# Performance work log

Hardware: AMD Instinct MI355X
Metric: run time of the kernel (lower is better)

Reference implementation:

```python
import jax, jax.numpy as jnp
import numpy as np

B, L, D = 64, 1024, 64  # (batch*heads, seq_len, head_dim)


def setup_inputs() -> dict:
    key = jax.random.key(0)
    kq, kk, kv = jax.random.split(key, 3)
    q = jax.random.normal(kq, (B, L, D), dtype=jnp.float32)
    k = jax.random.normal(kk, (B, L, D), dtype=jnp.float32)
    v = jax.random.normal(kv, (B, L, D), dtype=jnp.float32)
    scale = jnp.float32(1.0 / np.sqrt(D))  # standard 1/sqrt(d_head)
    return {"q": q, "k": k, "v": v, "scale": scale}


def reference(q, k, v, scale):
    # attention = bmm(q, k^T) * scale  -> [B, L, L]
    attention = jnp.einsum("bqd,bkd->bqk", q, k) * scale
    # softmax over dim=2 (keys); dropout p=0.0 is identity
    attention = jax.nn.softmax(attention, axis=2)
    # context = bmm(attention, v) -> [B, L, D]
    context = jnp.einsum("bqk,bkd->bqd", attention, v)
    return (context, attention)
```

## Files before the change

### kernel.cpp

```cpp
#include <hip/hip_runtime.h>
#include <hip/hip_bf16.h>

typedef __bf16 bf16x8 __attribute__((ext_vector_type(8)));
typedef float  f32x4  __attribute__((ext_vector_type(4)));

#define NB 64
#define LL 1024
#define DD 64
#define HK 512
#define PSTR 36

#define LSUM_LDS  (LL * DD * 2)
#define MAIN_LDS  (2 * HK * DD * 2 + 8 * 16 * PSTR * 4)

#define WS_VT_OFF 0
#define WS_RL_OFF ((size_t)8 * 1024 * 1024)
#define WS_NEED   (WS_RL_OFF + (size_t)NB * LL * 4)

#if __has_builtin(__builtin_amdgcn_exp2f)
#define EXP2(x) __builtin_amdgcn_exp2f(x)
#else
#define EXP2(x) exp2f(x)
#endif

__global__ __launch_bounds__(256)
void preconvert_v(const float* __restrict__ v, __bf16* __restrict__ vt) {
  const int blk = blockIdx.x, tid = threadIdx.x;
  const int b = blk >> 4, t = blk & 15;
  __shared__ float tile[64][65];
  const float* src = v + ((size_t)b * LL + t * 64) * DD;
  for (int i = tid; i < 64 * 16; i += 256) {
    const int row = i >> 4, c4 = (i & 15) * 4;
    f32x4 x = *(const f32x4*)(src + row * DD + c4);
    tile[row][c4 + 0] = x[0]; tile[row][c4 + 1] = x[1];
    tile[row][c4 + 2] = x[2]; tile[row][c4 + 3] = x[3];
  }
  __syncthreads();
  __bf16* dst = vt + (size_t)b * DD * LL + t * 64;
  for (int i = tid; i < 64 * 8; i += 256) {
    const int d = i >> 3, k8 = (i & 7) * 8;
    bf16x8 o;
    #pragma unroll
    for (int j = 0; j < 8; ++j) o[j] = (__bf16)tile[k8 + j][d];
    *(bf16x8*)(dst + (size_t)d * LL + k8) = o;
  }
}

__global__ __launch_bounds__(512, 1)
void lsum_kernel(const float* __restrict__ q, const float* __restrict__ kf,
                 const float* __restrict__ scale_p, float* __restrict__ rlbuf) {
  extern __shared__ char smem[];
  __bf16* Klds = (__bf16*)smem;

  const int tid  = threadIdx.x;
  const int lane = tid & 63;
  const int w    = tid >> 6;
  const int l15  = lane & 15;
  const int lg   = lane >> 4;

  int bid = blockIdx.x;
  bid = (bid & 7) * 32 + (bid >> 3);
  const int b     = bid >> 2;
  const int qrow0 = (bid & 3) * 256 + w * 32;

  const float scale2 = scale_p[0] * 1.4426950408889634f;
  const float* kb = kf + (size_t)b * LL * DD;

  #pragma unroll
  for (int it = 0; it < 16; ++it) {
    const int c = it * 512 + tid;
    const int row = c >> 3, slot = c & 7;
    const f32x4* s4 = (const f32x4*)(kb + (size_t)c * 8);
    f32x4 x0 = s4[0], x1 = s4[1];
    bf16x8 t;
    #pragma unroll
    for (int j = 0; j < 4; ++j) { t[j] = (__bf16)x0[j]; t[4 + j] = (__bf16)x1[j]; }
    *(bf16x8*)(Klds + row * 64 + ((slot * 8) ^ ((row & 7) * 8))) = t;
  }

  bf16x8 aq[2][2];
  #pragma unroll
  for (int u = 0; u < 2; ++u) {
    const float* qrow = q + ((size_t)b * LL + qrow0 + u * 16 + l15) * DD;
    #pragma unroll
    for (int s = 0; s < 2; ++s) {
      const f32x4* p4 = (const f32x4*)(qrow + s * 32 + lg * 8);
      f32x4 x0 = p4[0], x1 = p4[1];
      #pragma unroll
      for (int j = 0; j < 4; ++j) {
        aq[u][s][j]     = (__bf16)(x0[j] * scale2);
        aq[u][s][4 + j] = (__bf16)(x1[j] * scale2);
      }
    }
  }

  __syncthreads();

  const int xsw = (l15 & 7) * 8;
  float ls[2] = {0.f, 0.f};
  for (int kt = 0; kt < 32; ++kt) {
    bf16x8 bk[2][2];
    #pragma unroll
    for (int f = 0; f < 2; ++f)
      #pragma unroll
      for (int s = 0; s < 2; ++s)
        bk[f][s] = *(const bf16x8*)(Klds + (kt * 32 + f * 16 + l15) * 64
                                         + ((s * 32 + lg * 8) ^ xsw));
    #pragma unroll
    for (int u = 0; u < 2; ++u) {
      f32x4 sacc[2] = {{0.f,0.f,0.f,0.f},{0.f,0.f,0.f,0.f}};
      #pragma unroll
      for (int s = 0; s < 2; ++s)
        #pragma unroll
        for (int f = 0; f < 2; ++f)
          sacc[f] = __builtin_amdgcn_mfma_f32_16x16x32_bf16(bk[f][s], aq[u][s], sacc[f], 0, 0, 0);
      #pragma unroll
      for (int f = 0; f < 2; ++f)
        #pragma unroll
        for (int r = 0; r < 4; ++r)
          ls[u] += EXP2(sacc[f][r]);
    }
  }
  #pragma unroll
  for (int u = 0; u < 2; ++u) {
    ls[u] += __shfl_xor(ls[u], 16, 64);
    ls[u] += __shfl_xor(ls[u], 32, 64);
  }
  if (lg == 0) {
    float* rp = rlbuf + (size_t)b * LL + qrow0 + l15;
    rp[0]  = 1.0f / ls[0];
    rp[16] = 1.0f / ls[1];
  }
}

__global__ __launch_bounds__(512, 1)
void sdpa_store(const float* __restrict__ q, const float* __restrict__ kf,
                const __bf16* __restrict__ vt, const float* __restrict__ rlbuf,
                const float* __restrict__ scale_p, float* __restrict__ out) {
  extern __shared__ char smem[];
  __bf16* Klds = (__bf16*)smem;
  __bf16* Vlds = (__bf16*)(smem + HK * DD * 2);
  float*  Pw   = (float*)(smem + 2 * HK * DD * 2);

  const int tid  = threadIdx.x;
  const int lane = tid & 63;
  const int w    = tid >> 6;
  const int l15  = lane & 15;
  const int lg   = lane >> 4;

  int bid = blockIdx.x;
  bid = (bid & 7) * 32 + (bid >> 3);
  const int b     = bid >> 2;
  const int qrow0 = (bid & 3) * 256 + w * 32;

  const float scale2 = scale_p[0] * 1.4426950408889634f;
  const float* kb  = kf + (size_t)b * LL * DD;
  const __bf16* vb = vt + (size_t)b * DD * LL;
  float* ctxb  = out + ((size_t)b * LL + qrow0) * DD;
  float* attnb = out + (size_t)NB * LL * DD + (size_t)b * LL * LL
               + (size_t)qrow0 * LL;

  bf16x8 aq[2][2];
  #pragma unroll
  for (int u = 0; u < 2; ++u) {
    const float* qrow = q + ((size_t)b * LL + qrow0 + u * 16 + l15) * DD;
    #pragma unroll
    for (int s = 0; s < 2; ++s) {
      const f32x4* p4 = (const f32x4*)(qrow + s * 32 + lg * 8);
      f32x4 x0 = p4[0], x1 = p4[1];
      #pragma unroll
      for (int j = 0; j < 4; ++j) {
        aq[u][s][j]     = (__bf16)(x0[j] * scale2);
        aq[u][s][4 + j] = (__bf16)(x1[j] * scale2);
      }
    }
  }
  const float* rlp = rlbuf + (size_t)b * LL + qrow0 + l15;
  const float rl[2] = {rlp[0], rlp[16]};

  const int xsw = (l15 & 7) * 8;
  float* prow  = Pw + (w * 16 + l15) * PSTR;
  const int srl = lane >> 3;
  const int src8 = (lane & 7) * 4;
  const float* psr = Pw + (w * 16) * PSTR;

  f32x4 cacc[2][4];
  #pragma unroll
  for (int u = 0; u < 2; ++u)
    #pragma unroll
    for (int g = 0; g < 4; ++g)
      cacc[u][g] = (f32x4){0.f, 0.f, 0.f, 0.f};

  for (int h = 0; h < 2; ++h) {
    __syncthreads();
    #pragma unroll
    for (int it = 0; it < 8; ++it) {
      const int c = it * 512 + tid;
      const int row = c >> 3, slot = c & 7;
      const f32x4* s4 = (const f32x4*)(kb + ((size_t)(h * HK + row) * DD) + slot * 8);
      f32x4 x0 = s4[0], x1 = s4[1];
      bf16x8 t;
      #pragma unroll
      for (int j = 0; j < 4; ++j) { t[j] = (__bf16)x0[j]; t[4 + j] = (__bf16)x1[j]; }
      *(bf16x8*)(Klds + row * 64 + ((slot * 8) ^ ((row & 7) * 8))) = t;

      const int d = c >> 6, ks = c & 63;
      bf16x8 tv = *(const bf16x8*)(vb + (size_t)d * LL + h * HK + ks * 8);
      *(bf16x8*)(Vlds + d * HK + ((ks * 8) ^ ((d & 7) * 8))) = tv;
    }
    __syncthreads();

    for (int kt = 0; kt < HK / 32; ++kt) {
      bf16x8 bk[2][2];
      #pragma unroll
      for (int f = 0; f < 2; ++f)
        #pragma unroll
        for (int s = 0; s < 2; ++s)
          bk[f][s] = *(const bf16x8*)(Klds + (kt * 32 + f * 16 + l15) * 64
                                           + ((s * 32 + lg * 8) ^ xsw));
      bf16x8 bv[4];
      #pragma unroll
      for (int g = 0; g < 4; ++g)
        bv[g] = *(const bf16x8*)(Vlds + (g * 16 + l15) * HK
                                      + ((kt * 32 + lg * 8) ^ xsw));

      #pragma unroll
      for (int u = 0; u < 2; ++u) {
        f32x4 sacc[2] = {{0.f,0.f,0.f,0.f},{0.f,0.f,0.f,0.f}};
        #pragma unroll
        for (int s = 0; s < 2; ++s)
          #pragma unroll
          for (int f = 0; f < 2; ++f)
            sacc[f] = __builtin_amdgcn_mfma_f32_16x16x32_bf16(bk[f][s], aq[u][s], sacc[f], 0, 0, 0);

        #pragma unroll
        for (int f = 0; f < 2; ++f) {
          f32x4 pv;
          #pragma unroll
          for (int r = 0; r < 4; ++r)
            pv[r] = EXP2(sacc[f][r]) * rl[u];
          *(f32x4*)(prow + f * 16 + lg * 4) = pv;
        }

        f32x4 p0 = *(const f32x4*)(prow + lg * 8);
        f32x4 p1 = *(const f32x4*)(prow + lg * 8 + 4);
        bf16x8 pa;
        #pragma unroll
        for (int j = 0; j < 4; ++j) { pa[j] = (__bf16)p0[j]; pa[4 + j] = (__bf16)p1[j]; }
        #pragma unroll
        for (int g = 0; g < 4; ++g)
          cacc[u][g] = __builtin_amdgcn_mfma_f32_16x16x32_bf16(pa, bv[g], cacc[u][g], 0, 0, 0);

        #pragma unroll
        for (int j = 0; j < 2; ++j) {
          const int srow = j * 8 + srl;
          f32x4 sp = *(const f32x4*)(psr + srow * PSTR + src8);
          *(f32x4*)(attnb + (size_t)(u * 16 + srow) * LL
                          + h * HK + kt * 32 + src8) = sp;
        }
      }
    }
  }

  #pragma unroll
  for (int u = 0; u < 2; ++u)
    #pragma unroll
    for (int g = 0; g < 4; ++g)
      #pragma unroll
      for (int r = 0; r < 4; ++r)
        ctxb[(size_t)(u * 16 + lg * 4 + r) * DD + g * 16 + l15] = cacc[u][g][r];
}

#define BQ 64
#define BK 32
#define KSTRIDE 72
#define VSTRIDE 40
#define PSTRIDE 48

__global__ __launch_bounds__(256, 4)
void sdpa_fallback(const float* __restrict__ q, const float* __restrict__ k,
                   const float* __restrict__ v, const float* __restrict__ scale_p,
                   float* __restrict__ out) {
  const int tid  = threadIdx.x;
  const int lane = tid & 63;
  const int w    = tid >> 6;
  int bid = blockIdx.x;
  bid = (bid & 7) * 128 + (bid >> 3);
  const int b    = bid >> 4;
  const int qblk = (bid & 15) * BQ;

  __shared__ __bf16 Ks[BK * KSTRIDE];
  __shared__ __bf16 Vs[DD * VSTRIDE];
  __shared__ __bf16 Pp[4][16 * PSTRIDE];

  const float scale = scale_p[0];
  const float* qb = q + ((size_t)b * LL + qblk) * DD;
  const float* kb = k + (size_t)b * LL * DD;
  const float* vb = v + (size_t)b * LL * DD;
  float* ctx  = out + ((size_t)b * LL + qblk) * DD;
  float* attn = out + (size_t)NB * LL * DD + (size_t)b * LL * LL + (size_t)qblk * LL;

  const int l15 = lane & 15;
  const int lg  = lane >> 4;
  const int dchunk = lg * 8;

  bf16x8 aq[2];
  {
    const float* qrow = qb + (size_t)(w * 16 + l15) * DD;
    #pragma unroll
    for (int s = 0; s < 2; ++s) {
      const f32x4* p4 = (const f32x4*)(qrow + s * 32 + dchunk);
      f32x4 x0 = p4[0], x1 = p4[1];
      #pragma unroll
      for (int j = 0; j < 4; ++j) {
        aq[s][j]     = (__bf16)(x0[j] * scale);
        aq[s][4 + j] = (__bf16)(x1[j] * scale);
      }
    }
  }

  const int srow = tid >> 3;
  const int sd0  = (tid & 7) * 8;

  float lpart[4] = {0.f, 0.f, 0.f, 0.f};
  for (int kt = 0; kt < LL / BK; ++kt) {
    __syncthreads();
    {
      const f32x4* src = (const f32x4*)(kb + (size_t)(kt * BK + srow) * DD + sd0);
      f32x4 x0 = src[0], x1 = src[1];
      bf16x8 t;
      #pragma unroll
      for (int j = 0; j < 4; ++j) { t[j] = (__bf16)x0[j]; t[4 + j] = (__bf16)x1[j]; }
      *(bf16x8*)&Ks[srow * KSTRIDE + sd0] = t;
    }
    __syncthreads();
    f32x4 sacc[2] = {{0.f,0.f,0.f,0.f},{0.f,0.f,0.f,0.f}};
    #pragma unroll
    for (int s = 0; s < 2; ++s)
      #pragma unroll
      for (int f = 0; f < 2; ++f) {
        bf16x8 bk = *(const bf16x8*)&Ks[(f * 16 + l15) * KSTRIDE + s * 32 + dchunk];
        sacc[f] = __builtin_amdgcn_mfma_f32_16x16x32_bf16(aq[s], bk, sacc[f], 0, 0, 0);
      }
    #pragma unroll
    for (int f = 0; f < 2; ++f)
      #pragma unroll
      for (int r = 0; r < 4; ++r)
        lpart[r] += __expf(sacc[f][r]);
  }
  #pragma unroll
  for (int m = 1; m < 16; m <<= 1)
    #pragma unroll
    for (int r = 0; r < 4; ++r)
      lpart[r] += __shfl_xor(lpart[r], m, 64);
  float rl[4];
  #pragma unroll
  for (int r = 0; r < 4; ++r) rl[r] = 1.0f / lpart[r];

  f32x4 cacc[4] = {{0.f,0.f,0.f,0.f},{0.f,0.f,0.f,0.f},
                   {0.f,0.f,0.f,0.f},{0.f,0.f,0.f,0.f}};
  for (int kt = 0; kt < LL / BK; ++kt) {
    __syncthreads();
    {
      const f32x4* src = (const f32x4*)(kb + (size_t)(kt * BK + srow) * DD + sd0);
      f32x4 x0 = src[0], x1 = src[1];
      bf16x8 t;
      #pragma unroll
      for (int j = 0; j < 4; ++j) { t[j] = (__bf16)x0[j]; t[4 + j] = (__bf16)x1[j]; }
      *(bf16x8*)&Ks[srow * KSTRIDE + sd0] = t;
      const f32x4* vsrc = (const f32x4*)(vb + (size_t)(kt * BK + srow) * DD + sd0);
      f32x4 y0 = vsrc[0], y1 = vsrc[1];
      #pragma unroll
      for (int j = 0; j < 4; ++j) {
        Vs[(sd0 + j)     * VSTRIDE + srow] = (__bf16)y0[j];
        Vs[(sd0 + 4 + j) * VSTRIDE + srow] = (__bf16)y1[j];
      }
    }
    __syncthreads();
    f32x4 sacc[2] = {{0.f,0.f,0.f,0.f},{0.f,0.f,0.f,0.f}};
    #pragma unroll
    for (int s = 0; s < 2; ++s)
      #pragma unroll
      for (int f = 0; f < 2; ++f) {
        bf16x8 bk = *(const bf16x8*)&Ks[(f * 16 + l15) * KSTRIDE + s * 32 + dchunk];
        sacc[f] = __builtin_amdgcn_mfma_f32_16x16x32_bf16(aq[s], bk, sacc[f], 0, 0, 0);
      }
    #pragma unroll
    for (int f = 0; f < 2; ++f)
      #pragma unroll
      for (int r = 0; r < 4; ++r) {
        const int row = lg * 4 + r;
        float p = __expf(sacc[f][r]) * rl[r];
        attn[(size_t)(w * 16 + row) * LL + (kt * BK + f * 16 + l15)] = p;
        Pp[w][row * PSTRIDE + f * 16 + l15] = (__bf16)p;
      }
    bf16x8 pa = *(const bf16x8*)&Pp[w][l15 * PSTRIDE + lg * 8];
    #pragma unroll
    for (int g = 0; g < 4; ++g) {
      bf16x8 bv = *(const bf16x8*)&Vs[(g * 16 + l15) * VSTRIDE + lg * 8];
      cacc[g] = __builtin_amdgcn_mfma_f32_16x16x32_bf16(pa, bv, cacc[g], 0, 0, 0);
    }
  }
  #pragma unroll
  for (int g = 0; g < 4; ++g)
    #pragma unroll
    for (int r = 0; r < 4; ++r)
      ctx[(size_t)(w * 16 + lg * 4 + r) * DD + g * 16 + l15] = cacc[g][r];
}

extern "C" void kernel_launch(void* const* d_in, const int* in_sizes, int n_in,
                              void* d_out, int out_size, void* d_ws, size_t ws_size,
                              hipStream_t stream) {
  const float* q = (const float*)d_in[0];
  const float* k = (const float*)d_in[1];
  const float* v = (const float*)d_in[2];
  const float* s = (const float*)d_in[3];
  float* out = (float*)d_out;

  if (ws_size >= WS_NEED) {
    __bf16* vt = (__bf16*)((char*)d_ws + WS_VT_OFF);
    float*  rl = (float*)((char*)d_ws + WS_RL_OFF);
    preconvert_v<<<dim3(NB * (LL / 64)), dim3(256), 0, stream>>>(v, vt);
    (void)hipFuncSetAttribute((const void*)lsum_kernel,
                              hipFuncAttributeMaxDynamicSharedMemorySize, LSUM_LDS);
    lsum_kernel<<<dim3(256), dim3(512), LSUM_LDS, stream>>>(q, k, s, rl);
    (void)hipFuncSetAttribute((const void*)sdpa_store,
                              hipFuncAttributeMaxDynamicSharedMemorySize, MAIN_LDS);
    sdpa_store<<<dim3(256), dim3(512), MAIN_LDS, stream>>>(q, k, vt, rl, s, out);
  } else {
    sdpa_fallback<<<dim3(NB * (LL / 64)), dim3(256), 0, stream>>>(q, k, v, s, out);
  }
}
```

Measured before the change: 107.8 us.

## Split context and attention-store work across kernels with double-buffered row-wise stores

The row-sum kernel now also computes the context output, streaming V from global memory with a one-step register prefetch, so the second kernel no longer needs V. The second kernel only writes the attention matrix. All 8 waves cooperate on 8 query rows at a time, stage probabilities as bf16 in a double-buffered LDS tile, and each wave writes a full contiguous 512-float half-row per phase. The aim is more coalesced, streaming writes of the large attention output, decoupled from the PV matmul. The cost is that QK^T and exp are recomputed in both kernels, and the stored attention values are rounded through bf16.

```diff
diff --git a/kernel.cpp b/kernel.cpp
--- a/kernel.cpp
+++ b/kernel.cpp
@@ -2,16 +2,17 @@
 #include <hip/hip_bf16.h>
 
 typedef __bf16 bf16x8 __attribute__((ext_vector_type(8)));
+typedef __bf16 bf16x4 __attribute__((ext_vector_type(4)));
 typedef float  f32x4  __attribute__((ext_vector_type(4)));
 
 #define NB 64
 #define LL 1024
 #define DD 64
-#define HK 512
 #define PSTR 36
-
-#define LSUM_LDS  (LL * DD * 2)
-#define MAIN_LDS  (2 * HK * DD * 2 + 8 * 16 * PSTR * 4)
+#define PS 516
+
+#define B_LDS (LL * DD * 2 + 8 * 16 * PSTR * 4)
+#define C_LDS (LL * DD * 2 + 2 * 8 * PS * 2)
 
 #define WS_VT_OFF 0
 #define WS_RL_OFF ((size_t)8 * 1024 * 1024)
@@ -22,6 +23,13 @@
 #else
 #define EXP2(x) exp2f(x)
 #endif
+
+#define PHASE_BARRIER() do {                                   \
+  __builtin_amdgcn_sched_barrier(0);                           \
+  asm volatile("s_waitcnt lgkmcnt(0)" ::: "memory");           \
+  __builtin_amdgcn_s_barrier();                                \
+  __builtin_amdgcn_sched_barrier(0);                           \
+} while (0)
 
 __global__ __launch_bounds__(256)
 void preconvert_v(const float* __restrict__ v, __bf16* __restrict__ vt) {
@@ -47,10 +55,12 @@
 }
 
 __global__ __launch_bounds__(512, 1)
-void lsum_kernel(const float* __restrict__ q, const float* __restrict__ kf,
-                 const float* __restrict__ scale_p, float* __restrict__ rlbuf) {
+void sdpa_nostore(const float* __restrict__ q, const float* __restrict__ kf,
+                  const __bf16* __restrict__ vt, const float* __restrict__ scale_p,
+                  float* __restrict__ rlbuf, float* __restrict__ out) {
   extern __shared__ char smem[];
   __bf16* Klds = (__bf16*)smem;
+  float*  Pw   = (float*)(smem + LL * DD * 2);
 
   const int tid  = threadIdx.x;
   const int lane = tid & 63;
@@ -64,7 +74,9 @@
   const int qrow0 = (bid & 3) * 256 + w * 32;
 
   const float scale2 = scale_p[0] * 1.4426950408889634f;
-  const float* kb = kf + (size_t)b * LL * DD;
+  const float* kb  = kf + (size_t)b * LL * DD;
+  const __bf16* vb = vt + (size_t)b * DD * LL;
+  float* ctxb = out + ((size_t)b * LL + qrow0) * DD;
 
   #pragma unroll
   for (int it = 0; it < 16; ++it) {
@@ -97,6 +109,7 @@
   __syncthreads();
 
   const int xsw = (l15 & 7) * 8;
+
   float ls[2] = {0.f, 0.f};
   for (int kt = 0; kt < 32; ++kt) {
     bf16x8 bk[2][2];
@@ -126,91 +139,154 @@
     ls[u] += __shfl_xor(ls[u], 16, 64);
     ls[u] += __shfl_xor(ls[u], 32, 64);
   }
+  const float rl[2] = {1.0f / ls[0], 1.0f / ls[1]};
   if (lg == 0) {
     float* rp = rlbuf + (size_t)b * LL + qrow0 + l15;
-    rp[0]  = 1.0f / ls[0];
-    rp[16] = 1.0f / ls[1];
-  }
+    rp[0]  = rl[0];
+    rp[16] = rl[1];
+  }
+
+  f32x4 cacc[2][4];
+  #pragma unroll
+  for (int u = 0; u < 2; ++u)
+    #pragma unroll
+    for (int g = 0; g < 4; ++g)
+      cacc[u][g] = (f32x4){0.f, 0.f, 0.f, 0.f};
+
+  float* prow = Pw + (w * 16 + l15) * PSTR;
+
+  bf16x8 bvn[4];
+  #pragma unroll
+  for (int g = 0; g < 4; ++g)
+    bvn[g] = *(const bf16x8*)(vb + (size_t)(g * 16 + l15) * LL + lg * 8);
+
+  for (int kt = 0; kt < 32; ++kt) {
+    bf16x8 bvc[4];
+    #pragma unroll
+    for (int g = 0; g < 4; ++g) bvc[g] = bvn[g];
+    if (kt + 1 < 32) {
+      #pragma unroll
+      for (int g = 0; g < 4; ++g)
+        bvn[g] = *(const bf16x8*)(vb + (size_t)(g * 16 + l15) * LL
+                                     + (kt + 1) * 32 + lg * 8);
+    }
+    bf16x8 bk[2][2];
+    #pragma unroll
+    for (int f = 0; f < 2; ++f)
+      #pragma unroll
+      for (int s = 0; s < 2; ++s)
+        bk[f][s] = *(const bf16x8*)(Klds + (kt * 32 + f * 16 + l15) * 64
+                                         + ((s * 32 + lg * 8) ^ xsw));
+    #pragma unroll
+    for (int u = 0; u < 2; ++u) {
+      f32x4 sacc[2] = {{0.f,0.f,0.f,0.f},{0.f,0.f,0.f,0.f}};
+      #pragma unroll
+      for (int s = 0; s < 2; ++s)
+        #pragma unroll
+        for (int f = 0; f < 2; ++f)
+          sacc[f] = __builtin_amdgcn_mfma_f32_16x16x32_bf16(bk[f][s], aq[u][s], sacc[f], 0, 0, 0);
+      #pragma unroll
+      for (int f = 0; f < 2; ++f) {
+        f32x4 pv;
+        #pragma unroll
+        for (int r = 0; r < 4; ++r)
+          pv[r] = EXP2(sacc[f][r]) * rl[u];
+        *(f32x4*)(prow + f * 16 + lg * 4) = pv;
+      }
+      f32x4 p0 = *(const f32x4*)(prow + lg * 8);
+      f32x4 p1 = *(const f32x4*)(prow + lg * 8 + 4);
+      bf16x8 pa;
+      #pragma unroll
+      for (int j = 0; j < 4; ++j) { pa[j] = (__bf16)p0[j]; pa[4 + j] = (__bf16)p1[j]; }
+      #pragma unroll
+      for (int g = 0; g < 4; ++g)
+        cacc[u][g] = __builtin_amdgcn_mfma_f32_16x16x32_bf16(pa, bvc[g], cacc[u][g], 0, 0, 0);
+    }
+  }
+
+  #pragma unroll
+  for (int u = 0; u < 2; ++u)
+    #pragma unroll
+    for (int g = 0; g < 4; ++g)
+      #pragma unroll
+      for (int r = 0; r < 4; ++r)
+        ctxb[(size_t)(u * 16 + lg * 4 + r) * DD + g * 16 + l15] = cacc[u][g][r];
 }
 
 __global__ __launch_bounds__(512, 1)
-void sdpa_store(const float* __restrict__ q, const float* __restrict__ kf,
-                const __bf16* __restrict__ vt, const float* __restrict__ rlbuf,
-                const float* __restrict__ scale_p, float* __restrict__ out) {
+void sdpa_cstore(const float* __restrict__ q, const float* __restrict__ kf,
+                 const float* __restrict__ rlbuf, const float* __restrict__ scale_p,
+                 float* __restrict__ out) {
   extern __shared__ char smem[];
   __bf16* Klds = (__bf16*)smem;
-  __bf16* Vlds = (__bf16*)(smem + HK * DD * 2);
-  float*  Pw   = (float*)(smem + 2 * HK * DD * 2);
+  __bf16* Pdb  = (__bf16*)(smem + LL * DD * 2);
 
   const int tid  = threadIdx.x;
   const int lane = tid & 63;
   const int w    = tid >> 6;
   const int l15  = lane & 15;
   const int lg   = lane >> 4;
+  const int qr   = l15 & 7;
 
   int bid = blockIdx.x;
   bid = (bid & 7) * 32 + (bid >> 3);
   const int b     = bid >> 2;
-  const int qrow0 = (bid & 3) * 256 + w * 32;
+  const int qrow0 = (bid & 3) * 256;
 
   const float scale2 = scale_p[0] * 1.4426950408889634f;
-  const float* kb  = kf + (size_t)b * LL * DD;
-  const __bf16* vb = vt + (size_t)b * DD * LL;
-  float* ctxb  = out + ((size_t)b * LL + qrow0) * DD;
+  const float* kb = kf + (size_t)b * LL * DD;
   float* attnb = out + (size_t)NB * LL * DD + (size_t)b * LL * LL
                + (size_t)qrow0 * LL;
 
-  bf16x8 aq[2][2];
-  #pragma unroll
-  for (int u = 0; u < 2; ++u) {
-    const float* qrow = q + ((size_t)b * LL + qrow0 + u * 16 + l15) * DD;
-    #pragma unroll
-    for (int s = 0; s < 2; ++s) {
-      const f32x4* p4 = (const f32x4*)(qrow + s * 32 + lg * 8);
-      f32x4 x0 = p4[0], x1 = p4[1];
-      #pragma unroll
-      for (int j = 0; j < 4; ++j) {
-        aq[u][s][j]     = (__bf16)(x0[j] * scale2);
-        aq[u][s][4 + j] = (__bf16)(x1[j] * scale2);
-      }
-    }
-  }
-  const float* rlp = rlbuf + (size_t)b * LL + qrow0 + l15;
-  const float rl[2] = {rlp[0], rlp[16]};
-
-  const int xsw = (l15 & 7) * 8;
-  float* prow  = Pw + (w * 16 + l15) * PSTR;
-  const int srl = lane >> 3;
-  const int src8 = (lane & 7) * 4;
-  const float* psr = Pw + (w * 16) * PSTR;
-
-  f32x4 cacc[2][4];
-  #pragma unroll
-  for (int u = 0; u < 2; ++u)
-    #pragma unroll
-    for (int g = 0; g < 4; ++g)
-      cacc[u][g] = (f32x4){0.f, 0.f, 0.f, 0.f};
-
-  for (int h = 0; h < 2; ++h) {
-    __syncthreads();
-    #pragma unroll
-    for (int it = 0; it < 8; ++it) {
-      const int c = it * 512 + tid;
-      const int row = c >> 3, slot = c & 7;
-      const f32x4* s4 = (const f32x4*)(kb + ((size_t)(h * HK + row) * DD) + slot * 8);
-      f32x4 x0 = s4[0], x1 = s4[1];
-      bf16x8 t;
-      #pragma unroll
-      for (int j = 0; j < 4; ++j) { t[j] = (__bf16)x0[j]; t[4 + j] = (__bf16)x1[j]; }
-      *(bf16x8*)(Klds + row * 64 + ((slot * 8) ^ ((row & 7) * 8))) = t;
-
-      const int d = c >> 6, ks = c & 63;
-      bf16x8 tv = *(const bf16x8*)(vb + (size_t)d * LL + h * HK + ks * 8);
-      *(bf16x8*)(Vlds + d * HK + ((ks * 8) ^ ((d & 7) * 8))) = tv;
-    }
-    __syncthreads();
-
-    for (int kt = 0; kt < HK / 32; ++kt) {
+  #pragma unroll
+  for (int it = 0; it < 16; ++it) {
+    const int c = it * 512 + tid;
+    const int row = c >> 3, slot = c & 7;
+    const f32x4* s4 = (const f32x4*)(kb + (size_t)c * 8);
+    f32x4 x0 = s4[0], x1 = s4[1];
+    bf16x8 t;
+    #pragma unroll
+    for (int j = 0; j < 4; ++j) { t[j] = (__bf16)x0[j]; t[4 + j] = (__bf16)x1[j]; }
+    *(bf16x8*)(Klds + row * 64 + ((slot * 8) ^ ((row & 7) * 8))) = t;
+  }
+
+  const float* qbase  = q + ((size_t)b * LL + qrow0 + qr) * DD;
+  const float* rlbase = rlbuf + (size_t)b * LL + qrow0 + qr;
+
+  f32x4 qn[4];
+  #pragma unroll
+  for (int t2 = 0; t2 < 2; ++t2) {
+    qn[2 * t2]     = *(const f32x4*)(qbase + t2 * 32 + lg * 8);
+    qn[2 * t2 + 1] = *(const f32x4*)(qbase + t2 * 32 + lg * 8 + 4);
+  }
+  float rln = rlbase[0];
+
+  __syncthreads();
+
+  const int xsw = qr * 8;
+  int cur = 0;
+  bf16x8 aq[2];
+  float rl = 0.f;
+
+  for (int p = 0; p < 64; ++p) {
+    const int c = p >> 1, hk = p & 1;
+
+    if (hk == 0) {
+      #pragma unroll
+      for (int s = 0; s < 2; ++s)
+        #pragma unroll
+        for (int j = 0; j < 4; ++j) {
+          aq[s][j]     = (__bf16)(qn[2 * s][j] * scale2);
+          aq[s][4 + j] = (__bf16)(qn[2 * s + 1][j] * scale2);
+        }
+      rl = rln;
+    }
+
+    __bf16* pb = Pdb + cur * (8 * PS) + qr * PS;
+    #pragma unroll
+    for (int i = 0; i < 2; ++i) {
+      const int ktl = 2 * w + i;
+      const int kt  = hk * 16 + ktl;
       bf16x8 bk[2][2];
       #pragma unroll
       for (int f = 0; f < 2; ++f)
@@ -218,57 +294,50 @@
         for (int s = 0; s < 2; ++s)
           bk[f][s] = *(const bf16x8*)(Klds + (kt * 32 + f * 16 + l15) * 64
                                            + ((s * 32 + lg * 8) ^ xsw));
-      bf16x8 bv[4];
-      #pragma unroll
-      for (int g = 0; g < 4; ++g)
-        bv[g] = *(const bf16x8*)(Vlds + (g * 16 + l15) * HK
-                                      + ((kt * 32 + lg * 8) ^ xsw));
-
-      #pragma unroll
-      for (int u = 0; u < 2; ++u) {
-        f32x4 sacc[2] = {{0.f,0.f,0.f,0.f},{0.f,0.f,0.f,0.f}};
-        #pragma unroll
-        for (int s = 0; s < 2; ++s)
-          #pragma unroll
-          for (int f = 0; f < 2; ++f)
-            sacc[f] = __builtin_amdgcn_mfma_f32_16x16x32_bf16(bk[f][s], aq[u][s], sacc[f], 0, 0, 0);
-
-        #pragma unroll
-        for (int f = 0; f < 2; ++f) {
-          f32x4 pv;
-          #pragma unroll
-          for (int r = 0; r < 4; ++r)
-            pv[r] = EXP2(sacc[f][r]) * rl[u];
-          *(f32x4*)(prow + f * 16 + lg * 4) = pv;
-        }
-
-        f32x4 p0 = *(const f32x4*)(prow + lg * 8);
-        f32x4 p1 = *(const f32x4*)(prow + lg * 8 + 4);
-        bf16x8 pa;
-        #pragma unroll
-        for (int j = 0; j < 4; ++j) { pa[j] = (__bf16)p0[j]; pa[4 + j] = (__bf16)p1[j]; }
-        #pragma unroll
-        for (int g = 0; g < 4; ++g)
-          cacc[u][g] = __builtin_amdgcn_mfma_f32_16x16x32_bf16(pa, bv[g], cacc[u][g], 0, 0, 0);
-
-        #pragma unroll
-        for (int j = 0; j < 2; ++j) {
-          const int srow = j * 8 + srl;
-          f32x4 sp = *(const f32x4*)(psr + srow * PSTR + src8);
-          *(f32x4*)(attnb + (size_t)(u * 16 + srow) * LL
-                          + h * HK + kt * 32 + src8) = sp;
-        }
-      }
-    }
-  }
-
-  #pragma unroll
-  for (int u = 0; u < 2; ++u)
-    #pragma unroll
-    for (int g = 0; g < 4; ++g)
-      #pragma unroll
-      for (int r = 0; r < 4; ++r)
-        ctxb[(size_t)(u * 16 + lg * 4 + r) * DD + g * 16 + l15] = cacc[u][g][r];
+      f32x4 sacc[2] = {{0.f,0.f,0.f,0.f},{0.f,0.f,0.f,0.f}};
+      #pragma unroll
+      for (int s = 0; s < 2; ++s)
+        #pragma unroll
+        for (int f = 0; f < 2; ++f)
+          sacc[f] = __builtin_amdgcn_mfma_f32_16x16x32_bf16(bk[f][s], aq[s], sacc[f], 0, 0, 0);
+      #pragma unroll
+      for (int f = 0; f < 2; ++f) {
+        bf16x4 pv;
+        #pragma unroll
+        for (int r = 0; r < 4; ++r)
+          pv[r] = (__bf16)(EXP2(sacc[f][r]) * rl);
+        *(bf16x4*)(pb + ktl * 32 + f * 16 + lg * 4) = pv;
+      }
+    }
+
+    if (hk == 0 && c + 1 < 32) {
+      const float* qc = qbase + (size_t)(c + 1) * 8 * DD;
+      #pragma unroll
+      for (int t2 = 0; t2 < 2; ++t2) {
+        qn[2 * t2]     = *(const f32x4*)(qc + t2 * 32 + lg * 8);
+        qn[2 * t2 + 1] = *(const f32x4*)(qc + t2 * 32 + lg * 8 + 4);
+      }
+      rln = rlbase[(c + 1) * 8];
+    }
+
+    PHASE_BARRIER();
+
+    {
+      const __bf16* pr = Pdb + cur * (8 * PS) + w * PS;
+      float* arow = attnb + (size_t)(c * 8 + w) * LL + hk * 512;
+      #pragma unroll
+      for (int j = 0; j < 2; ++j) {
+        const uint2 rw = *(const uint2*)(pr + j * 256 + lane * 4);
+        f32x4 o;
+        o[0] = __uint_as_float(rw.x << 16);
+        o[1] = __uint_as_float(rw.x & 0xffff0000u);
+        o[2] = __uint_as_float(rw.y << 16);
+        o[3] = __uint_as_float(rw.y & 0xffff0000u);
+        *(f32x4*)(arow + j * 256 + lane * 4) = o;
+      }
+    }
+    cur ^= 1;
+  }
 }
 
 #define BQ 64
@@ -421,12 +490,12 @@
     __bf16* vt = (__bf16*)((char*)d_ws + WS_VT_OFF);
     float*  rl = (float*)((char*)d_ws + WS_RL_OFF);
     preconvert_v<<<dim3(NB * (LL / 64)), dim3(256), 0, stream>>>(v, vt);
-    (void)hipFuncSetAttribute((const void*)lsum_kernel,
-                              hipFuncAttributeMaxDynamicSharedMemorySize, LSUM_LDS);
-    lsum_kernel<<<dim3(256), dim3(512), LSUM_LDS, stream>>>(q, k, s, rl);
-    (void)hipFuncSetAttribute((const void*)sdpa_store,
-                              hipFuncAttributeMaxDynamicSharedMemorySize, MAIN_LDS);
-    sdpa_store<<<dim3(256), dim3(512), MAIN_LDS, stream>>>(q, k, vt, rl, s, out);
+    (void)hipFuncSetAttribute((const void*)sdpa_nostore,
+                              hipFuncAttributeMaxDynamicSharedMemorySize, B_LDS);
+    sdpa_nostore<<<dim3(256), dim3(512), B_LDS, stream>>>(q, k, vt, s, rl, out);
+    (void)hipFuncSetAttribute((const void*)sdpa_cstore,
+                              hipFuncAttributeMaxDynamicSharedMemorySize, C_LDS);
+    sdpa_cstore<<<dim3(256), dim3(512), C_LDS, stream>>>(q, k, rl, s, out);
   } else {
     sdpa_fallback<<<dim3(NB * (LL / 64)), dim3(256), 0, stream>>>(q, k, v, s, out);
   }
```

Measured after the change: 143.3 us. 1.33x slower.
